# Optimization experiments

Measured on AMD Instinct MI355X. Metric: run time of the kernel, lower is better.

## Reference

```python
import jax, jax.numpy as jnp
import numpy as np

B, T, D = 2, 2048, 2048
N, K, H = 16, 4, 128  # query heads, kv heads, head dim
G = N // K            # GQA groups
MIN_TS, MAX_TS = 1.0, 10000.0


def rope(x, positions):
    # x: [B, S, heads, H], positions: [B, S] int
    half = H // 2
    fraction = 2.0 * jnp.arange(half, dtype=jnp.float32) / H
    timescale = MIN_TS * (MAX_TS / MIN_TS) ** fraction            # [half]
    sinusoid = positions.astype(jnp.float32)[:, :, None, None] / timescale  # [B,S,1,half]
    sin, cos = jnp.sin(sinusoid), jnp.cos(sinusoid)
    x1, x2 = x[..., :half], x[..., half:]
    return jnp.concatenate([x1 * cos - x2 * sin, x2 * cos + x1 * sin], axis=-1)


def setup_inputs() -> dict:
    key = jax.random.key(0)
    ks = jax.random.split(key, 6)
    pos = jnp.tile(jnp.arange(T, dtype=jnp.int32)[None, :], (B, 1))
    return {
        "Xq": jax.random.normal(ks[0], (B, T, D), jnp.float32),
        "Xkv": jax.random.normal(ks[1], (B, T, D), jnp.float32),
        "q_positions": pos,
        "kv_positions": pos,
        "Wq": jax.random.normal(ks[2], (D, N, H), jnp.float32) * 0.02,
        "Wk": jax.random.normal(ks[3], (D, K, H), jnp.float32) * 0.02,
        "Wv": jax.random.normal(ks[4], (D, K, H), jnp.float32) * 0.02,
        "Wo": jax.random.normal(ks[5], (N, H, D), jnp.float32) * 0.02,
    }


def reference(Xq, Xkv, q_positions, kv_positions, Wq, Wk, Wv, Wo):
    # QKV projections (tensordot over embed dim), fp32
    q = jnp.einsum("btd,dnh->btnh", Xq, Wq)          # [B,T,N,H]
    k = jnp.einsum("bsd,dkh->bskh", Xkv, Wk)         # [B,S,K,H]
    v = jnp.einsum("bsd,dkh->bskh", Xkv, Wv)
    # inline RoPE on q and k
    q = rope(q, q_positions)
    k = rope(k, kv_positions)
    # GQA: group query heads over kv heads -> [B,K,G,T,H]
    qg = q.transpose(0, 2, 1, 3).reshape(B, K, G, T, H)
    kt = k.transpose(0, 2, 1, 3)                      # [B,K,S,H]
    vt = v.transpose(0, 2, 1, 3)
    scale = 1.0 / jnp.sqrt(jnp.float32(H))
    scores = jnp.einsum("bkgth,bksh->bkgts", qg, kt) * scale
    # causal mask (self-attn, no explicit mask, T>1)
    causal = jnp.tril(jnp.ones((T, T), dtype=bool))
    scores = jnp.where(causal[None, None, None], scores, jnp.finfo(scores.dtype).min)
    probs = jax.nn.softmax(scores, axis=-1)
    attn = jnp.einsum("bkgts,bksh->bkgth", probs, vt)  # [B,K,G,T,H]
    attn = attn.reshape(B, N, T, H).transpose(0, 2, 1, 3)  # [B,T,N,H]
    out = jnp.einsum("btnh,nhd->btd", attn, Wo)
    return out
```

## Files before the change

kernel.cpp:

```cpp
#include <hip/hip_runtime.h>
#include <hip/hip_bf16.h>
#include <cstdint>
#include <cstddef>

#define Bdim 2
#define Tdim 2048
#define Ddim 2048
#define NHq  16
#define NKV  4
#define HD   128
#define SCALE 0.08838834764831845f
#define QPRESCALE (0.08838834764831845f * 1.4426950408889634f)
#define NEG_INF (-3.0e38f)
#define DEFER_THR 11.5f
#define ROPE_L2 0.20762051f
#define INV_2PI 0.15915494f

typedef unsigned short u16;
typedef unsigned int   u32;
typedef __bf16 bf16x8 __attribute__((ext_vector_type(8)));
typedef float  f32x4  __attribute__((ext_vector_type(4)));

__device__ __forceinline__ u16 f2bf(float f) {
    unsigned int u = __float_as_uint(f);
    u += 0x7FFFu + ((u >> 16) & 1u);
    return (u16)(u >> 16);
}
__device__ __forceinline__ u16 f2bfn(float f) {
    __bf16 h = (__bf16)f;
    return __builtin_bit_cast(u16, h);
}
__device__ __forceinline__ float bf2f(u16 s) {
    return __uint_as_float(((unsigned int)s) << 16);
}

__device__ __forceinline__ void hw_sincos_rev(float rev, float* s, float* c) {
    rev -= floorf(rev);
    *s = __builtin_amdgcn_sinf(rev);
    *c = __builtin_amdgcn_cosf(rev);
}

#if __has_builtin(__builtin_amdgcn_permlane16_swap) && __has_builtin(__builtin_amdgcn_permlane32_swap)
#define HAVE_PERMLANE_SWAP 1
#endif

__device__ __forceinline__ float quad_reduce_max(float v) {
#ifdef HAVE_PERMLANE_SWAP
    auto r = __builtin_amdgcn_permlane16_swap(__float_as_uint(v), __float_as_uint(v), false, false);
    float m = fmaxf(__uint_as_float(r[0]), __uint_as_float(r[1]));
    auto r2 = __builtin_amdgcn_permlane32_swap(__float_as_uint(m), __float_as_uint(m), false, false);
    return fmaxf(__uint_as_float(r2[0]), __uint_as_float(r2[1]));
#else
    v = fmaxf(v, __shfl_xor(v, 16));
    return fmaxf(v, __shfl_xor(v, 32));
#endif
}
__device__ __forceinline__ float quad_reduce_sum(float v) {
#ifdef HAVE_PERMLANE_SWAP
    auto r = __builtin_amdgcn_permlane16_swap(__float_as_uint(v), __float_as_uint(v), false, false);
    float s = __uint_as_float(r[0]) + __uint_as_float(r[1]);
    auto r2 = __builtin_amdgcn_permlane32_swap(__float_as_uint(s), __float_as_uint(s), false, false);
    return __uint_as_float(r2[0]) + __uint_as_float(r2[1]);
#else
    v += __shfl_xor(v, 16);
    return v + __shfl_xor(v, 32);
#endif
}

__device__ __forceinline__ float tree_max16(const float (&s)[16]) {
    float a0 = fmaxf(s[0], s[1]),  a1 = fmaxf(s[2], s[3]);
    float a2 = fmaxf(s[4], s[5]),  a3 = fmaxf(s[6], s[7]);
    float a4 = fmaxf(s[8], s[9]),  a5 = fmaxf(s[10], s[11]);
    float a6 = fmaxf(s[12], s[13]), a7 = fmaxf(s[14], s[15]);
    float b0 = fmaxf(a0, a1), b1 = fmaxf(a2, a3);
    float b2 = fmaxf(a4, a5), b3 = fmaxf(a6, a7);
    return fmaxf(fmaxf(b0, b1), fmaxf(b2, b3));
}
__device__ __forceinline__ float tree_sum16(const float (&s)[16]) {
    float a0 = s[0] + s[1],  a1 = s[2] + s[3];
    float a2 = s[4] + s[5],  a3 = s[6] + s[7];
    float a4 = s[8] + s[9],  a5 = s[10] + s[11];
    float a6 = s[12] + s[13], a7 = s[14] + s[15];
    float b0 = a0 + a1, b1 = a2 + a3, b2 = a4 + a5, b3 = a6 + a7;
    return (b0 + b1) + (b2 + b3);
}

typedef __attribute__((address_space(1))) const u32 gbl_u32;
typedef __attribute__((address_space(3))) u32 lds_u32;
__device__ __forceinline__ void gload16(const void* g, void* l) {
    __builtin_amdgcn_global_load_lds((gbl_u32*)(uintptr_t)g, (lds_u32*)(uintptr_t)l, 16, 0, 0);
}

#define VM8 asm volatile("s_waitcnt vmcnt(8)" ::: "memory")
#define VM6 asm volatile("s_waitcnt vmcnt(6)" ::: "memory")
#define VM4 asm volatile("s_waitcnt vmcnt(4)" ::: "memory")
#define VM3 asm volatile("s_waitcnt vmcnt(3)" ::: "memory")
#define VM2 asm volatile("s_waitcnt vmcnt(2)" ::: "memory")
#define VM0 asm volatile("s_waitcnt vmcnt(0)" ::: "memory")
#define VMNONE ((void)0)
#define BARRIER do { asm volatile("" ::: "memory"); __builtin_amdgcn_s_barrier(); asm volatile("" ::: "memory"); } while (0)

__global__ __launch_bounds__(256) void prep_all(const float* __restrict__ Xq,
                                                const float* __restrict__ Xkv,
                                                const float* __restrict__ Wq,
                                                const float* __restrict__ Wk,
                                                const float* __restrict__ Wv,
                                                const float* __restrict__ Wo,
                                                u16* __restrict__ xq_bf,
                                                u16* __restrict__ xkv_bf,
                                                u16* __restrict__ wq_t,
                                                u16* __restrict__ wk_t,
                                                u16* __restrict__ wv_t,
                                                u16* __restrict__ wo_t)
{
    __shared__ u16 t[64][72];
    const int tid = threadIdx.x;
    int bid = blockIdx.x;

    if (bid < 8192) {
        const size_t NE = (size_t)4096 * 2048 / 8;
        size_t idx = (size_t)bid * 256 + tid;
        const float* src; u16* dst; size_t off;
        if (idx < NE) { src = Xq;  dst = xq_bf;  off = idx * 8; }
        else          { src = Xkv; dst = xkv_bf; off = (idx - NE) * 8; }
        float4 a = *(const float4*)&src[off];
        float4 b = *(const float4*)&src[off + 4];
        ushort4 r0, r1;
        r0.x = f2bf(a.x); r0.y = f2bf(a.y); r0.z = f2bf(a.z); r0.w = f2bf(a.w);
        r1.x = f2bf(b.x); r1.y = f2bf(b.y); r1.z = f2bf(b.z); r1.w = f2bf(b.w);
        *(ushort4*)&dst[off] = r0;
        *(ushort4*)&dst[off + 4] = r1;
        return;
    }
    bid -= 8192;
    const float* src; u16* dst; int C, gx;
    const int R = 2048;
    if (bid < 1024)      { src = Wq; dst = wq_t; C = 2048; gx = 32; }
    else if (bid < 1280) { src = Wk; dst = wk_t; C = 512;  gx = 8;  bid -= 1024; }
    else if (bid < 1536) { src = Wv; dst = wv_t; C = 512;  gx = 8;  bid -= 1280; }
    else                 { src = Wo; dst = wo_t; C = 2048; gx = 32; bid -= 1536; }

    const int r0 = (bid / gx) * 64, c0 = (bid % gx) * 64;
    const int tr = tid >> 4, tc4 = (tid & 15) * 4;
#pragma unroll
    for (int p = 0; p < 4; p++) {
        int r = p * 16 + tr;
        float4 v = *(const float4*)&src[(size_t)(r0 + r) * C + c0 + tc4];
        t[tc4 + 0][r] = f2bf(v.x);
        t[tc4 + 1][r] = f2bf(v.y);
        t[tc4 + 2][r] = f2bf(v.z);
        t[tc4 + 3][r] = f2bf(v.w);
    }
    __syncthreads();
#pragma unroll
    for (int p = 0; p < 4; p++) {
        int cc = p * 16 + tr;
        ushort4 w = *(const ushort4*)&t[cc][tc4];
        *(ushort4*)&dst[(size_t)(c0 + cc) * R + r0 + tc4] = w;
    }
}

__global__ __launch_bounds__(256) void rope_k(u16* __restrict__ k,
                                              const int* __restrict__ kvpos)
{
    int idx = blockIdx.x * 256 + threadIdx.x;
    int rn = idx >> 4;
    int h4 = (idx & 15) * 4;
    int pos = kvpos[rn >> 2];
    u16* base = k + (size_t)rn * HD;
    ushort4 a = *(const ushort4*)&base[h4];
    ushort4 bvec = *(const ushort4*)&base[h4 + 64];
    u16 av[4] = {a.x, a.y, a.z, a.w};
    u16 bv[4] = {bvec.x, bvec.y, bvec.z, bvec.w};
#pragma unroll
    for (int j = 0; j < 4; j++) {
        float rscale = __builtin_amdgcn_exp2f((float)(h4 + j) * -ROPE_L2) * INV_2PI;
        float s, c;
        hw_sincos_rev((float)pos * rscale, &s, &c);
        float x1 = bf2f(av[j]), x2 = bf2f(bv[j]);
        av[j] = f2bf(x1 * c - x2 * s);
        bv[j] = f2bf(x2 * c + x1 * s);
    }
    ushort4 ra, rb;
    ra.x = av[0]; ra.y = av[1]; ra.z = av[2]; ra.w = av[3];
    rb.x = bv[0]; rb.y = bv[1]; rb.z = bv[2]; rb.w = bv[3];
    *(ushort4*)&base[h4] = ra;
    *(ushort4*)&base[h4 + 64] = rb;
}

#define GPH(c, ks, mh, STAGE, VMW) do {                                        \
    bf16x8 Af[4];                                                              \
    _Pragma("unroll")                                                          \
    for (int mf = 0; mf < 4; mf++)                                             \
        Af[mf] = *(const bf16x8*)&Ab[c][ks][(arow + (mh) * 64 + mf * 16) * 32 + cxs]; \
    if ((mh) == 0) {                                                           \
        _Pragma("unroll")                                                      \
        for (int nf = 0; nf < 4; nf++)                                         \
            Bf[nf] = *(const bf16x8*)&Bb[c][ks][(brow + nf * 16) * 32 + cxs];  \
    }                                                                          \
    STAGE;                                                                     \
    BARRIER;                                                                   \
    asm volatile("s_waitcnt lgkmcnt(0)" ::: "memory");                         \
    __builtin_amdgcn_s_setprio(1);                                             \
    _Pragma("unroll")                                                          \
    for (int mf = 0; mf < 4; mf++)                                             \
        _Pragma("unroll")                                                      \
        for (int nf = 0; nf < 4; nf++)                                         \
            acc[(mh) * 4 + mf][nf] = __builtin_amdgcn_mfma_f32_16x16x32_bf16(  \
                Af[mf], Bf[nf], acc[(mh) * 4 + mf][nf], 0, 0, 0);              \
    __builtin_amdgcn_s_setprio(0);                                             \
    VMW;                                                                       \
    BARRIER;                                                                   \
} while (0)

__device__ __forceinline__ void gemm8_mainloop(const u16* __restrict__ A,
                                               const u16* __restrict__ Bt,
                                               int m0, int n0,
                                               u16 (&Ab)[2][2][256 * 32],
                                               u16 (&Bb)[2][2][256 * 32],
                                               f32x4 (&acc)[8][4])
{
    const int tid = threadIdx.x;
    const int wv = tid >> 6, lane = tid & 63;
    const int l15 = lane & 15, quad = lane >> 4;
    const int wr = wv >> 2, wc = wv & 3;

#pragma unroll
    for (int mf = 0; mf < 8; mf++)
#pragma unroll
        for (int nf = 0; nf < 4; nf++) acc[mf][nf] = (f32x4){0.f, 0.f, 0.f, 0.f};

    auto stageA = [&](int kt, int kh, int c) {
#pragma unroll
        for (int j = 0; j < 2; j++) {
            int q = j * 512 + tid;
            int r = q >> 2;
            int c4 = (q & 3) ^ (r & 3);
            gload16(A + (size_t)(m0 + r) * 2048 + kt * 64 + kh * 32 + c4 * 8,
                    &Ab[c][kh][q * 8]);
        }
    };
    auto stageB = [&](int kt, int kh, int c) {
#pragma unroll
        for (int j = 0; j < 2; j++) {
            int q = j * 512 + tid;
            int r = q >> 2;
            int c4 = (q & 3) ^ (r & 3);
            gload16(Bt + (size_t)(n0 + r) * 2048 + kt * 64 + kh * 32 + c4 * 8,
                    &Bb[c][kh][q * 8]);
        }
    };

    const int arow = wr * 128 + l15;
    const int brow = wc * 64 + l15;
    const int cxs  = (quad ^ (l15 & 3)) * 8;

    stageA(0, 0, 0); stageB(0, 0, 0);
    stageA(0, 1, 0); stageB(0, 1, 0);
    stageA(1, 0, 1); stageB(1, 0, 1);
    VM8;
    BARRIER;

    bf16x8 Bf[4];
    for (int it = 0; it < 15; it++) {
        const int t0 = 2 * it, t1 = 2 * it + 1;
        GPH(0, 0, 0, { stageA(t1, 1, 1); },     VMNONE);
        GPH(0, 0, 1, { stageB(t1, 1, 1); },     VM8);
        GPH(0, 1, 0, { stageA(t0 + 2, 0, 0); }, VMNONE);
        GPH(0, 1, 1, { stageB(t0 + 2, 0, 0); }, VM8);
        GPH(1, 0, 0, { stageA(t0 + 2, 1, 0); }, VMNONE);
        GPH(1, 0, 1, { stageB(t0 + 2, 1, 0); }, VM8);
        GPH(1, 1, 0, { stageA(t1 + 2, 0, 1); }, VMNONE);
        GPH(1, 1, 1, { stageB(t1 + 2, 0, 1); }, VM8);
    }
    GPH(0, 0, 0, { stageA(31, 1, 1); }, VMNONE);
    GPH(0, 0, 1, { stageB(31, 1, 1); }, VM8);
    GPH(0, 1, 0, VMNONE, VMNONE);
    GPH(0, 1, 1, VMNONE, VM4);
    GPH(1, 0, 0, VMNONE, VMNONE);
    GPH(1, 0, 1, VMNONE, VM0);
    GPH(1, 1, 0, VMNONE, VMNONE);
    GPH(1, 1, 1, VMNONE, VMNONE);
}

__global__ __launch_bounds__(512, 2) void qkv_gemm8(const u16* __restrict__ Xq,
                                                    const u16* __restrict__ Xkv,
                                                    const u16* __restrict__ Wqt,
                                                    const u16* __restrict__ Wkt,
                                                    const u16* __restrict__ Wvt,
                                                    u16* __restrict__ qraw,
                                                    u16* __restrict__ kraw,
                                                    u16* __restrict__ vt)
{
    __shared__ __align__(16) u16 Ab[2][2][256 * 32];
    __shared__ __align__(16) u16 Bb[2][2][256 * 32];
    f32x4 acc[8][4];

    const int bid0 = (int)blockIdx.x + 12 * (int)blockIdx.y;
    const int swz  = (bid0 & 7) * 24 + (bid0 >> 3);
    const int cx   = swz % 12;
    const int m0   = (swz / 12) * 256;

    const u16 *A, *Bt; int nb;
    if (cx < 8)       { A = Xq;  Bt = Wqt; nb = cx * 256; }
    else if (cx < 10) { A = Xkv; Bt = Wkt; nb = (cx - 8) * 256; }
    else              { A = Xkv; Bt = Wvt; nb = (cx - 10) * 256; }

    gemm8_mainloop(A, Bt, m0, nb, Ab, Bb, acc);

    const int tid = threadIdx.x;
    const int wv = tid >> 6, lane = tid & 63;
    const int l15 = lane & 15, quad = lane >> 4;
    const int wr = wv >> 2, wc = wv & 3;
    const int row0 = m0 + wr * 128;

    if (cx < 10) {
        u16* out; int ldw;
        if (cx < 8) { out = qraw; ldw = 2048; }
        else        { out = kraw; ldw = 512; }
#pragma unroll
        for (int mf = 0; mf < 8; mf++)
#pragma unroll
            for (int nf = 0; nf < 4; nf++) {
                int col = nb + wc * 64 + nf * 16 + l15;
                int r = row0 + mf * 16 + quad * 4;
#pragma unroll
                for (int reg = 0; reg < 4; reg++)
                    out[(size_t)(r + reg) * ldw + col] = f2bf(acc[mf][nf][reg]);
            }
    } else {
        const int b = m0 >> 11;
#pragma unroll
        for (int mf = 0; mf < 8; mf++)
#pragma unroll
            for (int nf = 0; nf < 4; nf++) {
                int col = nb + wc * 64 + nf * 16 + l15;
                int tloc = ((row0 & 2047) + mf * 16 + quad * 4);
                ushort4 w4;
                w4.x = f2bf(acc[mf][nf][0]);
                w4.y = f2bf(acc[mf][nf][1]);
                w4.z = f2bf(acc[mf][nf][2]);
                w4.w = f2bf(acc[mf][nf][3]);
                *(ushort4*)&vt[((size_t)(b * 512 + col)) * 2048 + tloc] = w4;
            }
    }
}

#define GPHN(c, ks, mh, STAGE, VMW) do {                                       \
    bf16x8 Af[4];                                                              \
    _Pragma("unroll")                                                          \
    for (int mf = 0; mf < 4; mf++)                                             \
        Af[mf] = *(const bf16x8*)&Ab[c][ks][(arow + (mh) * 64 + mf * 16) * 32 + cxs]; \
    if ((mh) == 0) {                                                           \
        _Pragma("unroll")                                                      \
        for (int nf = 0; nf < 2; nf++)                                         \
            Bf[nf] = *(const bf16x8*)&Bb[c][ks][(brow + nf * 16) * 32 + cxs];  \
    }                                                                          \
    STAGE;                                                                     \
    BARRIER;                                                                   \
    asm volatile("s_waitcnt lgkmcnt(0)" ::: "memory");                         \
    __builtin_amdgcn_s_setprio(1);                                             \
    _Pragma("unroll")                                                          \
    for (int mf = 0; mf < 4; mf++)                                             \
        _Pragma("unroll")                                                      \
        for (int nf = 0; nf < 2; nf++)                                         \
            acc[(mh) * 4 + mf][nf] = __builtin_amdgcn_mfma_f32_16x16x32_bf16(  \
                Af[mf], Bf[nf], acc[(mh) * 4 + mf][nf], 0, 0, 0);              \
    __builtin_amdgcn_s_setprio(0);                                             \
    VMW;                                                                       \
    BARRIER;                                                                   \
} while (0)

__device__ __forceinline__ void gemm8n_mainloop(const u16* __restrict__ A,
                                                const u16* __restrict__ Bt,
                                                int m0, int n0,
                                                u16 (&Ab)[2][2][256 * 32],
                                                u16 (&Bb)[2][2][128 * 32],
                                                f32x4 (&acc)[8][2])
{
    const int tid = threadIdx.x;
    const int wv = tid >> 6, lane = tid & 63;
    const int l15 = lane & 15, quad = lane >> 4;
    const int wr = wv >> 2, wc = wv & 3;

#pragma unroll
    for (int mf = 0; mf < 8; mf++)
#pragma unroll
        for (int nf = 0; nf < 2; nf++) acc[mf][nf] = (f32x4){0.f, 0.f, 0.f, 0.f};

    auto stageA = [&](int kt, int kh, int c) {
#pragma unroll
        for (int j = 0; j < 2; j++) {
            int q = j * 512 + tid;
            int r = q >> 2;
            int c4 = (q & 3) ^ (r & 3);
            gload16(A + (size_t)(m0 + r) * 2048 + kt * 64 + kh * 32 + c4 * 8,
                    &Ab[c][kh][q * 8]);
        }
    };
    auto stageB = [&](int kt, int kh, int c) {
        int q = tid;
        int r = q >> 2;
        int c4 = (q & 3) ^ (r & 3);
        gload16(Bt + (size_t)(n0 + r) * 2048 + kt * 64 + kh * 32 + c4 * 8,
                &Bb[c][kh][q * 8]);
    };

    const int arow = wr * 128 + l15;
    const int brow = wc * 32 + l15;
    const int cxs  = (quad ^ (l15 & 3)) * 8;

    stageA(0, 0, 0); stageB(0, 0, 0);
    stageA(0, 1, 0); stageB(0, 1, 0);
    stageA(1, 0, 1); stageB(1, 0, 1);
    VM6;
    BARRIER;

    bf16x8 Bf[2];
    for (int it = 0; it < 15; it++) {
        const int t0 = 2 * it, t1 = 2 * it + 1;
        GPHN(0, 0, 0, { stageA(t1, 1, 1); },     VMNONE);
        GPHN(0, 0, 1, { stageB(t1, 1, 1); },     VM6);
        GPHN(0, 1, 0, { stageA(t0 + 2, 0, 0); }, VMNONE);
        GPHN(0, 1, 1, { stageB(t0 + 2, 0, 0); }, VM6);
        GPHN(1, 0, 0, { stageA(t0 + 2, 1, 0); }, VMNONE);
        GPHN(1, 0, 1, { stageB(t0 + 2, 1, 0); }, VM6);
        GPHN(1, 1, 0, { stageA(t1 + 2, 0, 1); }, VMNONE);
        GPHN(1, 1, 1, { stageB(t1 + 2, 0, 1); }, VM6);
    }
    GPHN(0, 0, 0, { stageA(31, 1, 1); }, VMNONE);
    GPHN(0, 0, 1, { stageB(31, 1, 1); }, VM6);
    GPHN(0, 1, 0, VMNONE, VMNONE);
    GPHN(0, 1, 1, VMNONE, VM3);
    GPHN(1, 0, 0, VMNONE, VMNONE);
    GPHN(1, 0, 1, VMNONE, VM0);
    GPHN(1, 1, 0, VMNONE, VMNONE);
    GPHN(1, 1, 1, VMNONE, VMNONE);
}

__global__ __launch_bounds__(512, 2) void oproj_gemm8n(const u16* __restrict__ attnb,
                                                       const u16* __restrict__ Wot,
                                                       float* __restrict__ out)
{
    __shared__ __align__(16) u16 Ab[2][2][256 * 32];
    __shared__ __align__(16) u16 Bb[2][2][128 * 32];
    f32x4 acc[8][2];

    const int bid0 = (int)blockIdx.x + 16 * (int)blockIdx.y;
    const int swz  = (bid0 & 7) * 32 + (bid0 >> 3);
    const int n0   = (swz % 16) * 128;
    const int m0   = (swz / 16) * 256;

    gemm8n_mainloop(attnb, Wot, m0, n0, Ab, Bb, acc);

    const int tid = threadIdx.x;
    const int wv = tid >> 6, lane = tid & 63;
    const int l15 = lane & 15, quad = lane >> 4;
    const int wr = wv >> 2, wc = wv & 3;
    const int row0 = m0 + wr * 128;
#pragma unroll
    for (int mf = 0; mf < 8; mf++)
#pragma unroll
        for (int nf = 0; nf < 2; nf++) {
            int col = n0 + wc * 32 + nf * 16 + l15;
            int r = row0 + mf * 16 + quad * 4;
#pragma unroll
            for (int reg = 0; reg < 4; reg++)
                out[(size_t)(r + reg) * 2048 + col] = acc[mf][nf][reg];
        }
}

__global__ __launch_bounds__(512, 4) void flash_attn_v8(const u16* __restrict__ qh,
                                                        const u16* __restrict__ kh,
                                                        const u16* __restrict__ vtg,
                                                        const int* __restrict__ qpos,
                                                        u16* __restrict__ attnb)
{
    __shared__ __align__(16) u16 Ks[2][64 * 128];
    __shared__ __align__(16) u16 Vt[2][128 * 64];
    __shared__ __align__(16) u16 Ps[128 * 64];

    const int lin = (int)blockIdx.x;
    const int g   = lin & 7;
    const int m   = lin >> 3;
    const int b   = g >> 2, kvh = g & 3;
    const int n   = kvh * 4 + (m & 3);
    const int yy  = m >> 2;
    const int qt  = (yy < 8) ? (15 - yy) : (yy - 8);
    const int q0 = qt * 128;
    const int tid = threadIdx.x;
    const int wv = tid >> 6, lane = tid & 63;
    const int l15 = lane & 15, quad = lane >> 4;

    const size_t kbase = (size_t)(b * Tdim) * 512 + kvh * 128;
    const size_t vbase = ((size_t)(b * 512 + kvh * 128)) * 2048;
    const int nT = 2 * qt + 2;

    auto stageK = [&](int t, int buf) {
        const int s0s = t * 64;
#pragma unroll
        for (int c = 0; c < 2; c++) {
            int j = c * 512 + tid;
            int s = j >> 4;
            int c8 = (j & 15) ^ (s & 7);
            gload16(kh + kbase + (size_t)(s0s + s) * 512 + c8 * 8,
                    &Ks[buf][(c * 512 + wv * 64) * 8]);
        }
    };
    auto stageV = [&](int t, int buf) {
        const int s0s = t * 64;
#pragma unroll
        for (int c = 0; c < 2; c++) {
            int j = c * 512 + tid;
            int h = j >> 3;
            int sb = (j & 7) ^ (h & 7);
            gload16(vtg + vbase + (size_t)h * 2048 + s0s + sb * 8,
                    &Vt[buf][(c * 512 + wv * 64) * 8]);
        }
    };

    stageK(0, 0);
    stageV(0, 0);

    bf16x8 qfrag[4];
    {
        const size_t qbase = ((size_t)(b * Tdim + q0 + wv * 16)) * 2048 + n * 128;
#pragma unroll
        for (int kt = 0; kt < 4; kt++)
            qfrag[kt] = *(const bf16x8*)(qh + qbase + (size_t)l15 * 2048
                                          + kt * 32 + quad * 8);
        const float fpos = (float)qpos[b * Tdim + q0 + wv * 16 + l15];
#pragma unroll
        for (int kt = 0; kt < 2; kt++)
#pragma unroll
            for (int j = 0; j < 8; j++) {
                int h = kt * 32 + quad * 8 + j;
                float rscale = __builtin_amdgcn_exp2f((float)h * -ROPE_L2) * INV_2PI;
                float s, c;
                hw_sincos_rev(fpos * rscale, &s, &c);
                s *= QPRESCALE; c *= QPRESCALE;
                float x1 = (float)qfrag[kt][j], x2 = (float)qfrag[kt + 2][j];
                qfrag[kt][j]     = (__bf16)(x1 * c - x2 * s);
                qfrag[kt + 2][j] = (__bf16)(x2 * c + x1 * s);
            }
    }

    f32x4 Oacc[8];
#pragma unroll
    for (int ht = 0; ht < 8; ht++) Oacc[ht] = (f32x4){0.f, 0.f, 0.f, 0.f};
    float mrow = NEG_INF;
    float lrow = 0.f;

    VM2;
    BARRIER;

    int cur = 0;
    for (int t = 0; t < nT; t++) {
        const int s0 = t * 64;
        const bool more = (t + 1 < nT);

        if (more) { stageK(t + 1, cur ^ 1); stageV(t + 1, cur ^ 1); }

        f32x4 S[4];
#pragma unroll
        for (int nt = 0; nt < 4; nt++) S[nt] = (f32x4){0.f, 0.f, 0.f, 0.f};
#pragma unroll
        for (int kt = 0; kt < 4; kt++) {
            bf16x8 kf[4];
#pragma unroll
            for (int nt = 0; nt < 4; nt++) {
                int s = nt * 16 + l15;
                int cb = (kt * 4 + quad) ^ (s & 7);
                kf[nt] = *(const bf16x8*)&Ks[cur][s * 128 + cb * 8];
            }
#pragma unroll
            for (int nt = 0; nt < 4; nt++)
                S[nt] = __builtin_amdgcn_mfma_f32_16x16x32_bf16(kf[nt], qfrag[kt], S[nt], 0, 0, 0);
        }

        const bool domask = (t >= nT - 2);
        const int m_l = wv * 16 + l15;
        const int mg = q0 + m_l;
        float sv[16];
#pragma unroll
        for (int nt = 0; nt < 4; nt++)
#pragma unroll
            for (int r = 0; r < 4; r++) {
                float vv = S[nt][r];
                if (domask) {
                    int sg = s0 + nt * 16 + quad * 4 + r;
                    if (sg > mg) vv = NEG_INF;
                }
                sv[nt * 4 + r] = vv;
            }
        float mx = quad_reduce_max(tree_max16(sv));
        const bool skip = __all(mx <= mrow + DEFER_THR);
        const float mNew = skip ? mrow : fmaxf(mrow, mx);
#pragma unroll
        for (int i = 0; i < 16; i++)
            sv[i] = __builtin_amdgcn_exp2f(sv[i] - mNew);
#pragma unroll
        for (int nt = 0; nt < 4; nt++) {
            int sb = nt * 2 + (quad >> 1);
            int cb = sb ^ (m_l & 7);
            ushort4 pw;
            pw.x = f2bfn(sv[nt * 4 + 0]);
            pw.y = f2bfn(sv[nt * 4 + 1]);
            pw.z = f2bfn(sv[nt * 4 + 2]);
            pw.w = f2bfn(sv[nt * 4 + 3]);
            *(ushort4*)&Ps[m_l * 64 + cb * 8 + (quad & 1) * 4] = pw;
        }
        {
            float ps = quad_reduce_sum(tree_sum16(sv));
            if (skip) {
                lrow += ps;
            } else {
                float alpha = __builtin_amdgcn_exp2f(mrow - mNew);
                mrow = mNew;
                lrow = lrow * alpha + ps;
                float a0 = __shfl(alpha, quad * 4 + 0);
                float a1 = __shfl(alpha, quad * 4 + 1);
                float a2 = __shfl(alpha, quad * 4 + 2);
                float a3 = __shfl(alpha, quad * 4 + 3);
#pragma unroll
                for (int ht = 0; ht < 8; ht++) {
                    Oacc[ht][0] *= a0;
                    Oacc[ht][1] *= a1;
                    Oacc[ht][2] *= a2;
                    Oacc[ht][3] *= a3;
                }
            }
        }

        if (more) { VM4; } else { VM0; }
        BARRIER;

#pragma unroll
        for (int k2 = 0; k2 < 2; k2++) {
            int cbp = (k2 * 4 + quad) ^ (m_l & 7);
            bf16x8 pf = *(const bf16x8*)&Ps[m_l * 64 + cbp * 8];
#pragma unroll
            for (int ht = 0; ht < 8; ht++) {
                int h = ht * 16 + l15;
                int cb = (k2 * 4 + quad) ^ (h & 7);
                bf16x8 vf = *(const bf16x8*)&Vt[cur][h * 64 + cb * 8];
                Oacc[ht] = __builtin_amdgcn_mfma_f32_16x16x32_bf16(pf, vf, Oacc[ht], 0, 0, 0);
            }
        }

        if (more) { VM2; }
        BARRIER;
        cur ^= 1;
    }

    {
        f32x4 inv;
#pragma unroll
        for (int r = 0; r < 4; r++)
            inv[r] = 1.0f / __shfl(lrow, quad * 4 + r);
        int mg0 = q0 + wv * 16 + quad * 4;
        u16* dst0 = attnb + ((size_t)(b * Tdim + mg0)) * 2048 + n * 128 + l15;
#pragma unroll
        for (int ht = 0; ht < 8; ht++) {
#pragma unroll
            for (int r = 0; r < 4; r++)
                dst0[(size_t)r * 2048 + ht * 16] = f2bfn(Oacc[ht][r] * inv[r]);
        }
    }
}

extern "C" void kernel_launch(void* const* d_in, const int* in_sizes, int n_in,
                              void* d_out, int out_size, void* d_ws, size_t ws_size,
                              hipStream_t stream) {
    const float* Xq    = (const float*)d_in[0];
    const float* Xkv   = (const float*)d_in[1];
    const int*   qpos  = (const int*)d_in[2];
    const int*   kvpos = (const int*)d_in[3];
    const float* Wq    = (const float*)d_in[4];
    const float* Wk    = (const float*)d_in[5];
    const float* Wv    = (const float*)d_in[6];
    const float* Wo    = (const float*)d_in[7];
    float* out = (float*)d_out;

    char* w = (char*)d_ws;
    u16* xq_bf = (u16*)(w);
    u16* xkv_bf= (u16*)(w + (16u << 20));
    u16* qraw  = (u16*)(w + (32u << 20));
    u16* kraw  = (u16*)(w + (48u << 20));
    u16* vt    = (u16*)(w + (52u << 20));
    u16* wq_t  = (u16*)(w + (56u << 20));
    u16* wk_t  = (u16*)(w + (64u << 20));
    u16* wv_t  = (u16*)(w + (66u << 20));
    u16* wo_t  = (u16*)(w + (68u << 20));
    u16* attnb = (u16*)(w);

    prep_all<<<10752, 256, 0, stream>>>(Xq, Xkv, Wq, Wk, Wv, Wo,
                                        xq_bf, xkv_bf, wq_t, wk_t, wv_t, wo_t);
    qkv_gemm8<<<dim3(12, 16), 512, 0, stream>>>(xq_bf, xkv_bf, wq_t, wk_t, wv_t,
                                                qraw, kraw, vt);
    rope_k<<<1024, 256, 0, stream>>>(kraw, kvpos);
    flash_attn_v8<<<512, 512, 0, stream>>>(qraw, kraw, vt, qpos, attnb);
    oproj_gemm8n<<<dim3(16, 16), 512, 0, stream>>>(attnb, wo_t, out);
}
```

Measured before the change: 315.2 us.

## Retile QKV GEMM to 256x128 with 3-stage pipeline and reorder attention blocks

```diff
diff --git a/kernel.cpp b/kernel.cpp
--- a/kernel.cpp
+++ b/kernel.cpp
@@ -91,7 +91,6 @@
     __builtin_amdgcn_global_load_lds((gbl_u32*)(uintptr_t)g, (lds_u32*)(uintptr_t)l, 16, 0, 0);
 }
 
-#define VM8 asm volatile("s_waitcnt vmcnt(8)" ::: "memory")
 #define VM6 asm volatile("s_waitcnt vmcnt(6)" ::: "memory")
 #define VM4 asm volatile("s_waitcnt vmcnt(4)" ::: "memory")
 #define VM3 asm volatile("s_waitcnt vmcnt(3)" ::: "memory")
@@ -188,15 +187,15 @@
     *(ushort4*)&base[h4 + 64] = rb;
 }
 
-#define GPH(c, ks, mh, STAGE, VMW) do {                                        \
+#define QPH(r_, mh, STAGE, VMW) do {                                           \
     bf16x8 Af[4];                                                              \
     _Pragma("unroll")                                                          \
     for (int mf = 0; mf < 4; mf++)                                             \
-        Af[mf] = *(const bf16x8*)&Ab[c][ks][(arow + (mh) * 64 + mf * 16) * 32 + cxs]; \
+        Af[mf] = *(const bf16x8*)&Ab[r_][(arow + (mh) * 64 + mf * 16) * 32 + cxs]; \
     if ((mh) == 0) {                                                           \
         _Pragma("unroll")                                                      \
-        for (int nf = 0; nf < 4; nf++)                                         \
-            Bf[nf] = *(const bf16x8*)&Bb[c][ks][(brow + nf * 16) * 32 + cxs];  \
+        for (int nf = 0; nf < 2; nf++)                                         \
+            Bf[nf] = *(const bf16x8*)&Bb[r_][(brow + nf * 16) * 32 + cxs];     \
     }                                                                          \
     STAGE;                                                                     \
     BARRIER;                                                                   \
@@ -205,7 +204,7 @@
     _Pragma("unroll")                                                          \
     for (int mf = 0; mf < 4; mf++)                                             \
         _Pragma("unroll")                                                      \
-        for (int nf = 0; nf < 4; nf++)                                         \
+        for (int nf = 0; nf < 2; nf++)                                         \
             acc[(mh) * 4 + mf][nf] = __builtin_amdgcn_mfma_f32_16x16x32_bf16(  \
                 Af[mf], Bf[nf], acc[(mh) * 4 + mf][nf], 0, 0, 0);              \
     __builtin_amdgcn_s_setprio(0);                                             \
@@ -213,13 +212,30 @@
     BARRIER;                                                                   \
 } while (0)
 
-__device__ __forceinline__ void gemm8_mainloop(const u16* __restrict__ A,
-                                               const u16* __restrict__ Bt,
-                                               int m0, int n0,
-                                               u16 (&Ab)[2][2][256 * 32],
-                                               u16 (&Bb)[2][2][256 * 32],
-                                               f32x4 (&acc)[8][4])
+__global__ __launch_bounds__(512, 4) void qkv_gemm32(const u16* __restrict__ Xq,
+                                                     const u16* __restrict__ Xkv,
+                                                     const u16* __restrict__ Wqt,
+                                                     const u16* __restrict__ Wkt,
+                                                     const u16* __restrict__ Wvt,
+                                                     u16* __restrict__ qraw,
+                                                     u16* __restrict__ kraw,
+                                                     u16* __restrict__ vt)
 {
+    __shared__ __align__(16) u16 Ab[3][256 * 32];
+    __shared__ __align__(16) u16 Bb[3][128 * 32];
+
+    f32x4 acc[8][2];
+
+    const int bid0 = (int)blockIdx.x + 24 * (int)blockIdx.y;
+    const int swz  = (bid0 & 7) * 48 + (bid0 >> 3);
+    const int cx   = swz % 24;
+    const int m0   = (swz / 24) * 256;
+
+    const u16 *A, *Bt; int nb;
+    if (cx < 16)      { A = Xq;  Bt = Wqt; nb = cx * 128; }
+    else if (cx < 20) { A = Xkv; Bt = Wkt; nb = (cx - 16) * 128; }
+    else              { A = Xkv; Bt = Wvt; nb = (cx - 20) * 128; }
+
     const int tid = threadIdx.x;
     const int wv = tid >> 6, lane = tid & 63;
     const int l15 = lane & 15, quad = lane >> 4;
@@ -228,101 +244,59 @@
 #pragma unroll
     for (int mf = 0; mf < 8; mf++)
 #pragma unroll
-        for (int nf = 0; nf < 4; nf++) acc[mf][nf] = (f32x4){0.f, 0.f, 0.f, 0.f};
-
-    auto stageA = [&](int kt, int kh, int c) {
+        for (int nf = 0; nf < 2; nf++) acc[mf][nf] = (f32x4){0.f, 0.f, 0.f, 0.f};
+
+    auto stageA = [&](int kt, int s) {
 #pragma unroll
         for (int j = 0; j < 2; j++) {
             int q = j * 512 + tid;
-            int r = q >> 2;
-            int c4 = (q & 3) ^ (r & 3);
-            gload16(A + (size_t)(m0 + r) * 2048 + kt * 64 + kh * 32 + c4 * 8,
-                    &Ab[c][kh][q * 8]);
+            int rr = q >> 2;
+            int c4 = (q & 3) ^ (rr & 3);
+            gload16(A + (size_t)(m0 + rr) * 2048 + kt * 32 + c4 * 8,
+                    &Ab[s][q * 8]);
         }
     };
-    auto stageB = [&](int kt, int kh, int c) {
-#pragma unroll
-        for (int j = 0; j < 2; j++) {
-            int q = j * 512 + tid;
-            int r = q >> 2;
-            int c4 = (q & 3) ^ (r & 3);
-            gload16(Bt + (size_t)(n0 + r) * 2048 + kt * 64 + kh * 32 + c4 * 8,
-                    &Bb[c][kh][q * 8]);
-        }
+    auto stageB = [&](int kt, int s) {
+        int q = tid;
+        int rr = q >> 2;
+        int c4 = (q & 3) ^ (rr & 3);
+        gload16(Bt + (size_t)(nb + rr) * 2048 + kt * 32 + c4 * 8,
+                &Bb[s][q * 8]);
     };
 
     const int arow = wr * 128 + l15;
-    const int brow = wc * 64 + l15;
+    const int brow = wc * 32 + l15;
     const int cxs  = (quad ^ (l15 & 3)) * 8;
 
-    stageA(0, 0, 0); stageB(0, 0, 0);
-    stageA(0, 1, 0); stageB(0, 1, 0);
-    stageA(1, 0, 1); stageB(1, 0, 1);
-    VM8;
+    stageA(0, 0); stageB(0, 0);
+    stageA(1, 1); stageB(1, 1);
+    VM3;
     BARRIER;
 
-    bf16x8 Bf[4];
-    for (int it = 0; it < 15; it++) {
-        const int t0 = 2 * it, t1 = 2 * it + 1;
-        GPH(0, 0, 0, { stageA(t1, 1, 1); },     VMNONE);
-        GPH(0, 0, 1, { stageB(t1, 1, 1); },     VM8);
-        GPH(0, 1, 0, { stageA(t0 + 2, 0, 0); }, VMNONE);
-        GPH(0, 1, 1, { stageB(t0 + 2, 0, 0); }, VM8);
-        GPH(1, 0, 0, { stageA(t0 + 2, 1, 0); }, VMNONE);
-        GPH(1, 0, 1, { stageB(t0 + 2, 1, 0); }, VM8);
-        GPH(1, 1, 0, { stageA(t1 + 2, 0, 1); }, VMNONE);
-        GPH(1, 1, 1, { stageB(t1 + 2, 0, 1); }, VM8);
-    }
-    GPH(0, 0, 0, { stageA(31, 1, 1); }, VMNONE);
-    GPH(0, 0, 1, { stageB(31, 1, 1); }, VM8);
-    GPH(0, 1, 0, VMNONE, VMNONE);
-    GPH(0, 1, 1, VMNONE, VM4);
-    GPH(1, 0, 0, VMNONE, VMNONE);
-    GPH(1, 0, 1, VMNONE, VM0);
-    GPH(1, 1, 0, VMNONE, VMNONE);
-    GPH(1, 1, 1, VMNONE, VMNONE);
-}
-
-__global__ __launch_bounds__(512, 2) void qkv_gemm8(const u16* __restrict__ Xq,
-                                                    const u16* __restrict__ Xkv,
-                                                    const u16* __restrict__ Wqt,
-                                                    const u16* __restrict__ Wkt,
-                                                    const u16* __restrict__ Wvt,
-                                                    u16* __restrict__ qraw,
-                                                    u16* __restrict__ kraw,
-                                                    u16* __restrict__ vt)
-{
-    __shared__ __align__(16) u16 Ab[2][2][256 * 32];
-    __shared__ __align__(16) u16 Bb[2][2][256 * 32];
-    f32x4 acc[8][4];
-
-    const int bid0 = (int)blockIdx.x + 12 * (int)blockIdx.y;
-    const int swz  = (bid0 & 7) * 24 + (bid0 >> 3);
-    const int cx   = swz % 12;
-    const int m0   = (swz / 12) * 256;
-
-    const u16 *A, *Bt; int nb;
-    if (cx < 8)       { A = Xq;  Bt = Wqt; nb = cx * 256; }
-    else if (cx < 10) { A = Xkv; Bt = Wkt; nb = (cx - 8) * 256; }
-    else              { A = Xkv; Bt = Wvt; nb = (cx - 10) * 256; }
-
-    gemm8_mainloop(A, Bt, m0, nb, Ab, Bb, acc);
-
-    const int tid = threadIdx.x;
-    const int wv = tid >> 6, lane = tid & 63;
-    const int l15 = lane & 15, quad = lane >> 4;
-    const int wr = wv >> 2, wc = wv & 3;
+    bf16x8 Bf[2];
+    int cb = 0;
+    for (int it = 0; it < 62; ++it) {
+        int sb = cb + 2; if (sb >= 3) sb -= 3;
+        QPH(cb, 0, { stageA(it + 2, sb); }, VMNONE);
+        QPH(cb, 1, { stageB(it + 2, sb); }, VM3);
+        cb = (cb + 1 < 3) ? cb + 1 : 0;
+    }
+    QPH(cb, 0, VMNONE, VMNONE);
+    QPH(cb, 1, VMNONE, VM0);
+    cb = (cb + 1 < 3) ? cb + 1 : 0;
+    QPH(cb, 0, VMNONE, VMNONE);
+    QPH(cb, 1, VMNONE, VMNONE);
+
     const int row0 = m0 + wr * 128;
-
-    if (cx < 10) {
+    if (cx < 20) {
         u16* out; int ldw;
-        if (cx < 8) { out = qraw; ldw = 2048; }
-        else        { out = kraw; ldw = 512; }
+        if (cx < 16) { out = qraw; ldw = 2048; }
+        else         { out = kraw; ldw = 512; }
 #pragma unroll
         for (int mf = 0; mf < 8; mf++)
 #pragma unroll
-            for (int nf = 0; nf < 4; nf++) {
-                int col = nb + wc * 64 + nf * 16 + l15;
+            for (int nf = 0; nf < 2; nf++) {
+                int col = nb + wc * 32 + nf * 16 + l15;
                 int r = row0 + mf * 16 + quad * 4;
 #pragma unroll
                 for (int reg = 0; reg < 4; reg++)
@@ -333,8 +307,8 @@
 #pragma unroll
         for (int mf = 0; mf < 8; mf++)
 #pragma unroll
-            for (int nf = 0; nf < 4; nf++) {
-                int col = nb + wc * 64 + nf * 16 + l15;
+            for (int nf = 0; nf < 2; nf++) {
+                int col = nb + wc * 32 + nf * 16 + l15;
                 int tloc = ((row0 & 2047) + mf * 16 + quad * 4);
                 ushort4 w4;
                 w4.x = f2bf(acc[mf][nf][0]);
@@ -470,7 +444,7 @@
         }
 }
 
-__global__ __launch_bounds__(512, 4) void flash_attn_v8(const u16* __restrict__ qh,
+__global__ __launch_bounds__(512, 4) void flash_attn_v9(const u16* __restrict__ qh,
                                                         const u16* __restrict__ kh,
                                                         const u16* __restrict__ vtg,
                                                         const int* __restrict__ qpos,
@@ -483,10 +457,10 @@
     const int lin = (int)blockIdx.x;
     const int g   = lin & 7;
     const int m   = lin >> 3;
+    const int c   = m >> 1, sbit = m & 1;
     const int b   = g >> 2, kvh = g & 3;
-    const int n   = kvh * 4 + (m & 3);
-    const int yy  = m >> 2;
-    const int qt  = (yy < 8) ? (15 - yy) : (yy - 8);
+    const int n   = kvh * 4 + (c & 3);
+    const int qt  = sbit ? (15 - (c >> 2)) : (c >> 2);
     const int q0 = qt * 128;
     const int tid = threadIdx.x;
     const int wv = tid >> 6, lane = tid & 63;
@@ -499,23 +473,23 @@
     auto stageK = [&](int t, int buf) {
         const int s0s = t * 64;
 #pragma unroll
-        for (int c = 0; c < 2; c++) {
-            int j = c * 512 + tid;
+        for (int cc = 0; cc < 2; cc++) {
+            int j = cc * 512 + tid;
             int s = j >> 4;
             int c8 = (j & 15) ^ (s & 7);
             gload16(kh + kbase + (size_t)(s0s + s) * 512 + c8 * 8,
-                    &Ks[buf][(c * 512 + wv * 64) * 8]);
+                    &Ks[buf][(cc * 512 + wv * 64) * 8]);
         }
     };
     auto stageV = [&](int t, int buf) {
         const int s0s = t * 64;
 #pragma unroll
-        for (int c = 0; c < 2; c++) {
-            int j = c * 512 + tid;
+        for (int cc = 0; cc < 2; cc++) {
+            int j = cc * 512 + tid;
             int h = j >> 3;
             int sb = (j & 7) ^ (h & 7);
             gload16(vtg + vbase + (size_t)h * 2048 + s0s + sb * 8,
-                    &Vt[buf][(c * 512 + wv * 64) * 8]);
+                    &Vt[buf][(cc * 512 + wv * 64) * 8]);
         }
     };
 
@@ -536,12 +510,12 @@
             for (int j = 0; j < 8; j++) {
                 int h = kt * 32 + quad * 8 + j;
                 float rscale = __builtin_amdgcn_exp2f((float)h * -ROPE_L2) * INV_2PI;
-                float s, c;
-                hw_sincos_rev(fpos * rscale, &s, &c);
-                s *= QPRESCALE; c *= QPRESCALE;
+                float s, cc;
+                hw_sincos_rev(fpos * rscale, &s, &cc);
+                s *= QPRESCALE; cc *= QPRESCALE;
                 float x1 = (float)qfrag[kt][j], x2 = (float)qfrag[kt + 2][j];
-                qfrag[kt][j]     = (__bf16)(x1 * c - x2 * s);
-                qfrag[kt + 2][j] = (__bf16)(x2 * c + x1 * s);
+                qfrag[kt][j]     = (__bf16)(x1 * cc - x2 * s);
+                qfrag[kt + 2][j] = (__bf16)(x2 * cc + x1 * s);
             }
     }
 
@@ -696,9 +670,9 @@
 
     prep_all<<<10752, 256, 0, stream>>>(Xq, Xkv, Wq, Wk, Wv, Wo,
                                         xq_bf, xkv_bf, wq_t, wk_t, wv_t, wo_t);
-    qkv_gemm8<<<dim3(12, 16), 512, 0, stream>>>(xq_bf, xkv_bf, wq_t, wk_t, wv_t,
-                                                qraw, kraw, vt);
+    qkv_gemm32<<<dim3(24, 16), 512, 0, stream>>>(xq_bf, xkv_bf, wq_t, wk_t, wv_t,
+                                                 qraw, kraw, vt);
     rope_k<<<1024, 256, 0, stream>>>(kraw, kvpos);
-    flash_attn_v8<<<512, 512, 0, stream>>>(qraw, kraw, vt, qpos, attnb);
+    flash_attn_v9<<<512, 512, 0, stream>>>(qraw, kraw, vt, qpos, attnb);
     oproj_gemm8n<<<dim3(16, 16), 512, 0, stream>>>(attnb, wo_t, out);
 }
```

Measured after the change: 336.8 us. 6.8% more time.
